# Kernel optimization log

Hardware: AMD Instinct MI355X
Metric: run time of the kernel (lower is better)

## Reference

```python
import jax, jax.numpy as jnp
import numpy as np

B, C, H, W = 16, 512, 64, 64
WS = 16            # window size -> N = 256 tokens per window
NH = 16            # num heads, head_dim = 32
HD = C // NH
HID = int((4 * C * 0.5) / 64) * 64   # SwiGLU hidden = 1024
CPB = 512
EPS = 1e-5


def _rel_tables(ws):
    r = np.arange(-(ws - 1), ws, dtype=np.float32)
    tab = np.stack(np.meshgrid(r, r, indexing='ij'), axis=-1)  # (2ws-1,2ws-1,2)
    tab = tab / (ws - 1)
    tab = tab * 8.0
    tab = np.sign(tab) * np.log2(np.abs(tab) + 1.0) / np.log2(8.0)
    # relative position index (N,N)
    coords = np.stack(np.meshgrid(np.arange(ws), np.arange(ws), indexing='ij'))
    cf = coords.reshape(2, -1)
    rel = (cf[:, :, None] - cf[:, None, :]).transpose(1, 2, 0).astype(np.int64)
    rel[:, :, 0] += ws - 1
    rel[:, :, 1] += ws - 1
    rel[:, :, 0] *= 2 * ws - 1
    idx = rel.sum(-1)
    return tab.reshape(-1, 2), idx


def setup_inputs() -> dict:
    key = jax.random.key(0)
    ks = jax.random.split(key, 12)
    s = 0.02
    tab, idx = _rel_tables(WS)
    return {
        'x': jax.random.normal(ks[0], (B, C, H, W), jnp.float32),
        'rel_table': jnp.asarray(tab),
        'norm1_w': jnp.ones((C,), jnp.float32),
        'norm1_b': jnp.zeros((C,), jnp.float32),
        'norm2_w': jnp.ones((C,), jnp.float32),
        'norm2_b': jnp.zeros((C,), jnp.float32),
        'qkv_w': jax.random.normal(ks[1], (C, 3 * C), jnp.float32) * s,
        'proj_w': jax.random.normal(ks[2], (C, C), jnp.float32) * s,
        'cpb_w1': jax.random.normal(ks[3], (2, CPB), jnp.float32) * s,
        'cpb_b1': jnp.zeros((CPB,), jnp.float32),
        'cpb_w2': jax.random.normal(ks[4], (CPB, NH), jnp.float32) * s,
        'fc1_w': jax.random.normal(ks[5], (C, 2 * HID), jnp.float32) * s,
        'fc2_w': jax.random.normal(ks[6], (HID, C), jnp.float32) * s,
        'rel_index': jnp.asarray(idx),
    }


def _ln(x, w, b):
    m = jnp.mean(x, axis=-1, keepdims=True)
    v = jnp.mean(jnp.square(x - m), axis=-1, keepdims=True)
    return (x - m) * jax.lax.rsqrt(v + EPS) * w + b


def reference(x, rel_table, norm1_w, norm1_b, norm2_w, norm2_b, qkv_w, proj_w,
              cpb_w1, cpb_b1, cpb_w2, fc1_w, fc2_w, rel_index):
    ws, nh, hd = WS, NH, HD
    N = ws * ws
    # window partition: (B,C,H,W) -> (B*nW, N, C)
    xw = x.reshape(B, C, H // ws, ws, W // ws, ws)
    xw = xw.transpose(0, 2, 4, 3, 5, 1).reshape(-1, N, C)
    Bw = xw.shape[0]

    # --- window attention ---
    h = _ln(xw, norm1_w, norm1_b)
    qkv = (h @ qkv_w).reshape(Bw, N, 3, nh, hd).transpose(2, 0, 3, 1, 4)
    q, k, v = qkv[0], qkv[1], qkv[2]          # (Bw, nh, N, hd)
    attn = jnp.einsum('bhnd,bhmd->bhnm', q, k) * (hd ** -0.5)
    # Swin-v2 continuous position bias MLP + gather
    bias_tab = jax.nn.relu(rel_table @ cpb_w1 + cpb_b1) @ cpb_w2   # ((2ws-1)^2, nh)
    bias = bias_tab[rel_index]                 # (N, N, nh)
    bias = 16.0 * jax.nn.sigmoid(bias.transpose(2, 0, 1))          # (nh, N, N)
    attn = jax.nn.softmax(attn + bias[None], axis=-1)
    o = jnp.einsum('bhnm,bhmd->bhnd', attn, v)
    o = o.transpose(0, 2, 1, 3).reshape(Bw, N, C) @ proj_w
    xw = xw + o

    # --- SwiGLU MLP ---
    h2 = _ln(xw, norm2_w, norm2_b)
    u = h2 @ fc1_w
    val, gate = jnp.split(u, 2, axis=-1)       # Mlp/SwiGLU: chunk -> silu(gate)*x
    xw = xw + (jax.nn.silu(gate) * val) @ fc2_w

    # window reverse + outer skip
    xr = xw.reshape(B, H // ws, W // ws, ws, ws, C)
    xr = xr.transpose(0, 5, 1, 3, 2, 4).reshape(B, C, H, W)
    return xr + x
```

## Files before the change

### kernel.cpp

```cpp
#include <hip/hip_runtime.h>
#include <hip/hip_bf16.h>

typedef unsigned short u16;
typedef unsigned int u32;
typedef __attribute__((ext_vector_type(8))) u16 u16x8;
typedef __attribute__((ext_vector_type(4))) u16 u16x4;
typedef __attribute__((ext_vector_type(8))) short bf16x8;
typedef __attribute__((ext_vector_type(4))) float f32x4;

__device__ __forceinline__ u16 f2bf(float f) {
  u32 u = __float_as_uint(f);
  u += 0x7fffu + ((u >> 16) & 1u);
  return (u16)(u >> 16);
}
__device__ __forceinline__ float bf2f(u16 h) {
  return __uint_as_float(((u32)h) << 16);
}
__device__ __forceinline__ u16 cvt_bf(float f) {
  __hip_bfloat16 h(f);
  return __builtin_bit_cast(u16, h);
}
__device__ __forceinline__ bf16x8 ld_bf8(const u16* p) {
  return __builtin_bit_cast(bf16x8, *(const u16x8*)p);
}

#if __has_builtin(__builtin_amdgcn_exp2f)
#define EXP2(x) __builtin_amdgcn_exp2f(x)
#else
#define EXP2(x) exp2f(x)
#endif

typedef const void __attribute__((address_space(1)))* gas_t;
typedef void __attribute__((address_space(3)))* las_t;
#define GLOAD_LDS16(gp, lp) __builtin_amdgcn_global_load_lds((gas_t)(gp), (las_t)(lp), 16, 0, 0)

#define QSCALE 0.25503486f
#define BIAS_MUL 23.08312065f

__global__ void wtrans_kernel(const float* __restrict__ in, u16* __restrict__ out, int K, int N) {
  int idx = blockIdx.x * 256 + threadIdx.x;
  if (idx >= K * N) return;
  int n = idx / K, k = idx - n * K;
  out[idx] = f2bf(in[(size_t)k * N + n]);
}

__global__ void wtrans_fc1_kernel(const float* __restrict__ in, u16* __restrict__ out) {
  int idx = blockIdx.x * 256 + threadIdx.x;
  int n = idx >> 9, k = idx & 511;
  int i = ((n >> 5) << 4) | (n & 15);
  int gsel = (n >> 4) & 1;
  out[idx] = f2bf(in[(size_t)k * 2048 + i + gsel * 1024]);
}

__global__ void cpb_kernel(const float* __restrict__ rt, const float* __restrict__ w1,
                           const float* __restrict__ b1, const float* __restrict__ w2,
                           float* __restrict__ tab2) {
  __shared__ float hid[512];
  __shared__ float part[16][17];
  int tix = blockIdx.x;
  int t = threadIdx.x;
  float r0 = rt[tix * 2], r1 = rt[tix * 2 + 1];
  for (int j = t; j < 512; j += 256) {
    float v = r0 * w1[j] + r1 * w1[512 + j] + b1[j];
    hid[j] = v > 0.f ? v : 0.f;
  }
  __syncthreads();
  int hh = t & 15, seg = t >> 4;
  float acc = 0.f;
  for (int j = seg * 32; j < seg * 32 + 32; ++j) acc += hid[j] * w2[j * 16 + hh];
  part[seg][hh] = acc;
  __syncthreads();
  if (t < 16) {
    float s = 0.f;
    for (int g = 0; g < 16; ++g) s += part[g][t];
    tab2[t * 961 + tix] = BIAS_MUL / (1.f + __expf(-s)) - 23.0f;
  }
}

__global__ __launch_bounds__(256, 2) void ln1_kernel(
    const float* __restrict__ x, const float* __restrict__ w, const float* __restrict__ b,
    u16* __restrict__ hbuf, u16* __restrict__ xwbuf) {
  __shared__ u16 tile[512 * 33];
  __shared__ float red[2][8][32];
  __shared__ float meanv[32], rstdv[32];
  int bi = blockIdx.x;
  int bimg = bi >> 7, rest = bi & 127, hrow = rest >> 1, half = rest & 1;
  int t = threadIdx.x, p = t & 31, g = t >> 5;
  const float* xr = x + (size_t)bimg * 512 * 4096 + (size_t)hrow * 64 + half * 32;
  float s = 0.f, s2 = 0.f;
  for (int i = 0; i < 64; ++i) {
    int c = g * 64 + i;
    float v = xr[(size_t)c * 4096 + p];
    tile[c * 33 + p] = f2bf(v);
    s += v; s2 += v * v;
  }
  red[0][g][p] = s; red[1][g][p] = s2;
  __syncthreads();
  if (t < 32) {
    float ss = 0.f, qq = 0.f;
    for (int gg = 0; gg < 8; ++gg) { ss += red[0][gg][t]; qq += red[1][gg][t]; }
    float mu = ss * (1.f / 512.f);
    float var = qq * (1.f / 512.f) - mu * mu;
    meanv[t] = mu;
    rstdv[t] = rsqrtf(var + 1e-5f);
  }
  __syncthreads();
  int c0 = t * 2;
  float w0 = w[c0], w1v = w[c0 + 1], b0 = b[c0], b1v = b[c0 + 1];
  int hy = hrow >> 4, iy = hrow & 15;
  for (int pp = 0; pp < 32; ++pp) {
    int pixel = half * 32 + pp;
    int wx = pixel >> 4, ix = pixel & 15;
    int widx = bimg * 16 + hy * 4 + wx;
    size_t basep = ((size_t)widx * 256 + iy * 16 + ix) * 512;
    u16 rb0 = tile[c0 * 33 + pp], rb1 = tile[(c0 + 1) * 33 + pp];
    float mu = meanv[pp], rs = rstdv[pp];
    float v0 = bf2f(rb0), v1 = bf2f(rb1);
    *(u32*)(xwbuf + basep + c0) = (u32)rb0 | ((u32)rb1 << 16);
    u16 h0 = f2bf((v0 - mu) * rs * w0 + b0);
    u16 h1 = f2bf((v1 - mu) * rs * w1v + b1v);
    *(u32*)(hbuf + basep + c0) = (u32)h0 | ((u32)h1 << 16);
  }
}

template <int EPI>
__global__ __launch_bounds__(256, 4) void gemm_bt(
    const u16* __restrict__ A, const u16* __restrict__ Bt,
    u16* __restrict__ out, const u16* __restrict__ res,
    u16* __restrict__ q_o, u16* __restrict__ k_o, u16* __restrict__ v_o,
    int M, int N, int K) {
  __shared__ u16 As[128 * 64];
  __shared__ u16 Bs[128 * 64];
  const int t = threadIdx.x, l = t & 63, wv = t >> 6;
  const int nbx = N >> 7;
  const int wg = (int)blockIdx.x;
  const int xcd = wg & 7, c = wg >> 3;
  const int cm = c / nbx;
  const int m0 = (xcd * 64 + cm) * 128, n0 = (c - cm * nbx) * 128;
  const int wr = wv >> 1, wc = wv & 1;
  const int lr = l & 15, lk = l >> 4;
  f32x4 acc[4][4] = {};
  for (int kt = 0; kt < K; kt += 64) {
#pragma unroll
    for (int j = 0; j < 4; ++j) {
      int qi = j * 256 + t;
      int r = qi >> 3, c8 = (qi & 7) * 8;
      GLOAD_LDS16(A + (size_t)(m0 + r) * K + kt + c8, As + (size_t)(j * 256 + wv * 64) * 8);
    }
#pragma unroll
    for (int j = 0; j < 4; ++j) {
      int qi = j * 256 + t;
      int r = qi >> 3, c8 = (qi & 7) * 8;
      GLOAD_LDS16(Bt + (size_t)(n0 + r) * K + kt + c8, Bs + (size_t)(j * 256 + wv * 64) * 8);
    }
    __syncthreads();
#pragma unroll
    for (int ks = 0; ks < 2; ++ks) {
      bf16x8 a[4], bb[4];
#pragma unroll
      for (int mf = 0; mf < 4; ++mf)
        a[mf] = ld_bf8(As + (wr * 64 + mf * 16 + lr) * 64 + ks * 32 + lk * 8);
#pragma unroll
      for (int nf = 0; nf < 4; ++nf)
        bb[nf] = ld_bf8(Bs + (wc * 64 + nf * 16 + lr) * 64 + ks * 32 + lk * 8);
#pragma unroll
      for (int mf = 0; mf < 4; ++mf)
#pragma unroll
        for (int nf = 0; nf < 4; ++nf)
          acc[mf][nf] = __builtin_amdgcn_mfma_f32_16x16x32_bf16(a[mf], bb[nf], acc[mf][nf], 0, 0, 0);
    }
    __syncthreads();
  }
#pragma unroll
  for (int mf = 0; mf < 4; ++mf) {
    int rbase = m0 + wr * 64 + mf * 16 + lk * 4;
    if constexpr (EPI == 3) {
#pragma unroll
      for (int nf = 0; nf < 4; nf += 2) {
        int colv = n0 + wc * 64 + nf * 16 + lr;
        int i = ((colv >> 5) << 4) | (colv & 15);
#pragma unroll
        for (int jj = 0; jj < 4; ++jj) {
          int row = rbase + jj;
          float val = acc[mf][nf][jj], gate = acc[mf][nf + 1][jj];
          float sil = gate / (1.f + __expf(-gate));
          out[(size_t)row * 1024 + i] = f2bf(sil * val);
        }
      }
    } else {
#pragma unroll
      for (int nf = 0; nf < 4; ++nf) {
        int col = n0 + wc * 64 + nf * 16 + lr;
#pragma unroll
        for (int jj = 0; jj < 4; ++jj) {
          int row = rbase + jj;
          float v = acc[mf][nf][jj];
          if constexpr (EPI == 0) {
            out[(size_t)row * N + col] = f2bf(v);
          } else if constexpr (EPI == 1) {
            out[(size_t)row * N + col] = f2bf(v + bf2f(res[(size_t)row * N + col]));
          } else if constexpr (EPI == 2) {
            int which = col >> 9, rem = col & 511;
            int hh = rem >> 5, dd = rem & 31;
            size_t dst = (((size_t)(row >> 8) * 16 + hh) * 256 + (size_t)(row & 255)) * 32 + dd;
            u16* po = which == 0 ? q_o : (which == 1 ? k_o : v_o);
            float sc = which == 0 ? QSCALE : 1.f;
            po[dst] = f2bf(v * sc);
          }
        }
      }
    }
  }
}

__global__ __launch_bounds__(256, 4) void attn_kernel(
    const u16* __restrict__ qb, const u16* __restrict__ kb, const u16* __restrict__ vb,
    const float* __restrict__ tab2, u16* __restrict__ ob) {
  __shared__ u16 vt[32 * 72];
  __shared__ float tabh4[31 * 32 * 4];
  __shared__ u16 pl[4][16 * 76];
  const int w = blockIdx.x, h = blockIdx.y;
  const int t = threadIdx.x, l = t & 63, wid = t >> 6;
  const size_t base = (size_t)(w * 16 + h) * 256 * 32;
  const u16* qg = qb + base;
  const u16* kg = kb + base;
  const u16* vg = vb + base;
  const float* th = tab2 + h * 961;
  for (int i = t; i < 992; i += 256) {
    int dy = i >> 5, dx = i & 31;
#pragma unroll
    for (int r = 0; r < 4; ++r) {
      int dxr = dx + r;
      tabh4[i * 4 + r] = (dxr <= 30) ? th[dy * 31 + dxr] : 0.f;
    }
  }
  const int q4 = l >> 4, c0 = l & 15;
  const int dx0 = q4 * 4 - c0 + 15;
  bf16x8 qa[4];
#pragma unroll
  for (int mf = 0; mf < 4; ++mf)
    qa[mf] = ld_bf8(qg + (wid * 64 + mf * 16 + c0) * 32 + q4 * 8);
  f32x4 oacc[4][2] = {};
  float psum[4][4] = {};
  for (int ct = 0; ct < 4; ++ct) {
    {
      int r = t & 63, j = t >> 6;
      u16x8 dv = *(const u16x8*)(vg + (ct * 64 + r) * 32 + j * 8);
#pragma unroll
      for (int e = 0; e < 8; ++e) vt[(j * 8 + e) * 72 + r] = dv[e];
    }
    __syncthreads();
    bf16x8 bfr[4];
#pragma unroll
    for (int nf = 0; nf < 4; ++nf)
      bfr[nf] = ld_bf8(kg + (ct * 64 + nf * 16 + c0) * 32 + q4 * 8);
    bf16x8 vfr[2][2];
#pragma unroll
    for (int df = 0; df < 2; ++df)
#pragma unroll
      for (int ks2 = 0; ks2 < 2; ++ks2)
        vfr[df][ks2] = ld_bf8(vt + (df * 16 + c0) * 72 + ks2 * 32 + q4 * 8);
#pragma unroll
    for (int mf = 0; mf < 4; ++mf) {
      f32x4 sacc[4] = {};
      __builtin_amdgcn_s_setprio(1);
#pragma unroll
      for (int nf = 0; nf < 4; ++nf)
        sacc[nf] = __builtin_amdgcn_mfma_f32_16x16x32_bf16(qa[mf], bfr[nf], sacc[nf], 0, 0, 0);
      __builtin_amdgcn_s_setprio(0);
      const int dyb = wid * 4 + mf - ct * 4 + 15;
#pragma unroll
      for (int nf = 0; nf < 4; ++nf) {
        f32x4 bv = *(const f32x4*)&tabh4[((dyb - nf) * 32 + dx0) * 4];
#pragma unroll
        for (int jj = 0; jj < 4; ++jj) {
          float p = EXP2(sacc[nf][jj] + bv[jj]);
          psum[mf][jj] += p;
          pl[wid][(q4 * 4 + jj) * 76 + nf * 16 + c0] = cvt_bf(p);
        }
      }
      __builtin_amdgcn_s_setprio(1);
#pragma unroll
      for (int ks2 = 0; ks2 < 2; ++ks2) {
        bf16x8 pa = ld_bf8(&pl[wid][c0 * 76 + ks2 * 32 + q4 * 8]);
        oacc[mf][0] = __builtin_amdgcn_mfma_f32_16x16x32_bf16(pa, vfr[0][ks2], oacc[mf][0], 0, 0, 0);
        oacc[mf][1] = __builtin_amdgcn_mfma_f32_16x16x32_bf16(pa, vfr[1][ks2], oacc[mf][1], 0, 0, 0);
      }
      __builtin_amdgcn_s_setprio(0);
    }
    __syncthreads();
  }
#pragma unroll
  for (int mf = 0; mf < 4; ++mf) {
#pragma unroll
    for (int jj = 0; jj < 4; ++jj) {
      float s = psum[mf][jj];
      s += __shfl_xor(s, 1);
      s += __shfl_xor(s, 2);
      s += __shfl_xor(s, 4);
      s += __shfl_xor(s, 8);
      float inv = 1.f / s;
      int row = wid * 64 + mf * 16 + q4 * 4 + jj;
      size_t obase = ((size_t)w * 256 + row) * 512 + h * 32;
      ob[obase + c0] = f2bf(oacc[mf][0][jj] * inv);
      ob[obase + 16 + c0] = f2bf(oacc[mf][1][jj] * inv);
    }
  }
}

__global__ __launch_bounds__(256, 4) void ln2_kernel(const u16* __restrict__ r1,
    const float* __restrict__ w, const float* __restrict__ b, u16* __restrict__ h2) {
  int t = threadIdx.x, l = t & 63, wid = t >> 6;
  size_t token = (size_t)blockIdx.x * 4 + wid;
  const u16* rp = r1 + token * 512 + l * 8;
  u16x8 raw = *(const u16x8*)rp;
  float v[8]; float s = 0.f, s2 = 0.f;
#pragma unroll
  for (int i = 0; i < 8; ++i) { v[i] = bf2f(raw[i]); s += v[i]; s2 += v[i] * v[i]; }
#pragma unroll
  for (int m = 1; m < 64; m <<= 1) { s += __shfl_xor(s, m); s2 += __shfl_xor(s2, m); }
  float mu = s * (1.f / 512.f);
  float var = s2 * (1.f / 512.f) - mu * mu;
  float rs = rsqrtf(var + 1e-5f);
  u16x8 o;
#pragma unroll
  for (int i = 0; i < 8; ++i) {
    int c = l * 8 + i;
    o[i] = f2bf((v[i] - mu) * rs * w[c] + b[c]);
  }
  *(u16x8*)(h2 + token * 512 + l * 8) = o;
}

__global__ __launch_bounds__(256, 2) void final_kernel(const u16* __restrict__ r2,
    const float* __restrict__ x, float* __restrict__ out) {
  __shared__ u16 tl[64 * 132];
  int cc = blockIdx.x;
  int hrow = blockIdx.y;
  int bimg = blockIdx.z;
  int t = threadIdx.x;
  int p = t >> 2, cp = t & 3;
  int hy = hrow >> 4, iy = hrow & 15;
  {
    int wx = p >> 4, ix = p & 15;
    size_t token = (size_t)(bimg * 16 + hy * 4 + wx) * 256 + iy * 16 + ix;
    const u16* rp = r2 + token * 512 + cc * 128 + cp * 32;
#pragma unroll
    for (int i = 0; i < 4; ++i) {
      u16x8 d = *(const u16x8*)(rp + i * 8);
      *(u16x4*)(tl + p * 132 + cp * 32 + i * 8) = *(u16x4*)&d;
      *(u16x4*)(tl + p * 132 + cp * 32 + i * 8 + 4) = *((u16x4*)&d + 1);
    }
  }
  __syncthreads();
  int p2 = t & 63, cg = t >> 6;
  size_t pbase = (size_t)bimg * 512 * 4096 + (size_t)(cc * 128) * 4096 + (size_t)hrow * 64 + p2;
  const float* xp = x + pbase;
  float* op = out + pbase;
#pragma unroll
  for (int i = 0; i < 32; ++i) {
    int cl = cg * 32 + i;
    op[(size_t)cl * 4096] = bf2f(tl[p2 * 132 + cl]) + xp[(size_t)cl * 4096];
  }
}

extern "C" void kernel_launch(void* const* d_in, const int* in_sizes, int n_in,
                              void* d_out, int out_size, void* d_ws, size_t ws_size,
                              hipStream_t stream) {
  (void)in_sizes; (void)n_in; (void)out_size; (void)ws_size;
  const float* x = (const float*)d_in[0];
  const float* rel_table = (const float*)d_in[1];
  const float* n1w = (const float*)d_in[2];
  const float* n1b = (const float*)d_in[3];
  const float* n2w = (const float*)d_in[4];
  const float* n2b = (const float*)d_in[5];
  const float* qkv_w = (const float*)d_in[6];
  const float* proj_w = (const float*)d_in[7];
  const float* cpb_w1 = (const float*)d_in[8];
  const float* cpb_b1 = (const float*)d_in[9];
  const float* cpb_w2 = (const float*)d_in[10];
  const float* fc1_w = (const float*)d_in[11];
  const float* fc2_w = (const float*)d_in[12];
  float* outp = (float*)d_out;
  char* ws = (char*)d_ws;

  u16* wq = (u16*)(ws + 0);
  u16* wp = (u16*)(ws + 1572864);
  u16* w1 = (u16*)(ws + 2097152);
  u16* w2 = (u16*)(ws + 4194304);
  float* tab2 = (float*)(ws + 5242880);
  const size_t RB = 67108864;
  u16* R0 = (u16*)(ws + 8388608);
  u16* R1 = (u16*)(ws + 8388608 + RB);
  u16* R2 = (u16*)(ws + 8388608 + 2 * RB);
  u16* R3 = (u16*)(ws + 8388608 + 3 * RB);
  u16* R4 = (u16*)(ws + 8388608 + 4 * RB);
  u16* R5 = (u16*)(ws + 8388608 + 5 * RB);

  wtrans_kernel<<<3072, 256, 0, stream>>>(qkv_w, wq, 512, 1536);
  wtrans_kernel<<<1024, 256, 0, stream>>>(proj_w, wp, 512, 512);
  wtrans_fc1_kernel<<<4096, 256, 0, stream>>>(fc1_w, w1);
  wtrans_kernel<<<2048, 256, 0, stream>>>(fc2_w, w2, 1024, 512);
  cpb_kernel<<<961, 256, 0, stream>>>(rel_table, cpb_w1, cpb_b1, cpb_w2, tab2);
  ln1_kernel<<<2048, 256, 0, stream>>>(x, n1w, n1b, R2, R0);
  gemm_bt<2><<<6144, 256, 0, stream>>>(R2, wq, nullptr, nullptr,
                                       R3, R4, R5, 65536, 1536, 512);
  attn_kernel<<<dim3(256, 16), 256, 0, stream>>>(R3, R4, R5, tab2, R2);
  gemm_bt<1><<<2048, 256, 0, stream>>>(R2, wp, R1, R0,
                                       nullptr, nullptr, nullptr, 65536, 512, 512);
  ln2_kernel<<<16384, 256, 0, stream>>>(R1, n2w, n2b, R3);
  gemm_bt<3><<<8192, 256, 0, stream>>>(R3, w1, R4, nullptr,
                                       nullptr, nullptr, nullptr, 65536, 2048, 512);
  gemm_bt<1><<<2048, 256, 0, stream>>>(R4, w2, R0, R1,
                                       nullptr, nullptr, nullptr, 65536, 512, 1024);
  final_kernel<<<dim3(4, 64, 16), 256, 0, stream>>>(R0, x, outp);
}
```

Before: 806.9 us.

## Add double-buffered LDS GEMM for fc1 SwiGLU and raise attention occupancy

Introduces a new gemm_db kernel that stages A and B tiles into two LDS buffers with direct global-to-LDS loads, prefetching the tile two steps ahead while computing on the current one. It uses partial vmcnt waits and raised MFMA priority, and is used only for the fc1 GEMM with the fused SwiGLU epilogue. The attention kernel's launch bounds also change from 4 to 5 waves per SIMD hint. The extra LDS (64KB per block) limits occupancy to about 2 blocks per CU, and the tighter register cap on attention could cause spills.

```diff
diff --git a/kernel.cpp b/kernel.cpp
--- a/kernel.cpp
+++ b/kernel.cpp
@@ -213,7 +213,106 @@
   }
 }
 
-__global__ __launch_bounds__(256, 4) void attn_kernel(
+template <int EPI>
+__global__ __launch_bounds__(256, 2) void gemm_db(
+    const u16* __restrict__ A, const u16* __restrict__ Bt,
+    u16* __restrict__ out, const u16* __restrict__ res,
+    int M, int N, int K) {
+  __shared__ u16 As[2][128 * 64];
+  __shared__ u16 Bs[2][128 * 64];
+  const int t = threadIdx.x, l = t & 63, wv = t >> 6;
+  const int nbx = N >> 7;
+  const int wg = (int)blockIdx.x;
+  const int xcd = wg & 7, c = wg >> 3;
+  const int cm = c / nbx;
+  const int m0 = (xcd * 64 + cm) * 128, n0 = (c - cm * nbx) * 128;
+  const int wr = wv >> 1, wc = wv & 1;
+  const int lr = l & 15, lk = l >> 4;
+  const int nt = K >> 6;
+
+  auto stage = [&](int b, int kt) {
+#pragma unroll
+    for (int j = 0; j < 4; ++j) {
+      int qi = j * 256 + t;
+      int r = qi >> 3, c8 = (qi & 7) * 8;
+      GLOAD_LDS16(A + (size_t)(m0 + r) * K + kt + c8, &As[b][(size_t)(j * 256 + wv * 64) * 8]);
+    }
+#pragma unroll
+    for (int j = 0; j < 4; ++j) {
+      int qi = j * 256 + t;
+      int r = qi >> 3, c8 = (qi & 7) * 8;
+      GLOAD_LDS16(Bt + (size_t)(n0 + r) * K + kt + c8, &Bs[b][(size_t)(j * 256 + wv * 64) * 8]);
+    }
+  };
+
+  f32x4 acc[4][4] = {};
+  stage(0, 0);
+  stage(1, 64);
+  for (int tt = 0; tt < nt; ++tt) {
+    if (tt + 1 < nt)
+      asm volatile("s_waitcnt vmcnt(8)" ::: "memory");
+    else
+      asm volatile("s_waitcnt vmcnt(0)" ::: "memory");
+    __builtin_amdgcn_s_barrier();
+    const u16* as = &As[tt & 1][0];
+    const u16* bs = &Bs[tt & 1][0];
+#pragma unroll
+    for (int ks = 0; ks < 2; ++ks) {
+      bf16x8 a[4], bb[4];
+#pragma unroll
+      for (int mf = 0; mf < 4; ++mf)
+        a[mf] = ld_bf8(as + (wr * 64 + mf * 16 + lr) * 64 + ks * 32 + lk * 8);
+#pragma unroll
+      for (int nf = 0; nf < 4; ++nf)
+        bb[nf] = ld_bf8(bs + (wc * 64 + nf * 16 + lr) * 64 + ks * 32 + lk * 8);
+      __builtin_amdgcn_s_setprio(1);
+#pragma unroll
+      for (int mf = 0; mf < 4; ++mf)
+#pragma unroll
+        for (int nf = 0; nf < 4; ++nf)
+          acc[mf][nf] = __builtin_amdgcn_mfma_f32_16x16x32_bf16(a[mf], bb[nf], acc[mf][nf], 0, 0, 0);
+      __builtin_amdgcn_s_setprio(0);
+    }
+    asm volatile("s_waitcnt lgkmcnt(0)" ::: "memory");
+    __builtin_amdgcn_s_barrier();
+    if (tt + 2 < nt) stage(tt & 1, (tt + 2) * 64);
+  }
+#pragma unroll
+  for (int mf = 0; mf < 4; ++mf) {
+    int rbase = m0 + wr * 64 + mf * 16 + lk * 4;
+    if constexpr (EPI == 3) {
+#pragma unroll
+      for (int nf = 0; nf < 4; nf += 2) {
+        int colv = n0 + wc * 64 + nf * 16 + lr;
+        int i = ((colv >> 5) << 4) | (colv & 15);
+#pragma unroll
+        for (int jj = 0; jj < 4; ++jj) {
+          int row = rbase + jj;
+          float val = acc[mf][nf][jj], gate = acc[mf][nf + 1][jj];
+          float sil = gate / (1.f + __expf(-gate));
+          out[(size_t)row * 1024 + i] = f2bf(sil * val);
+        }
+      }
+    } else {
+#pragma unroll
+      for (int nf = 0; nf < 4; ++nf) {
+        int col = n0 + wc * 64 + nf * 16 + lr;
+#pragma unroll
+        for (int jj = 0; jj < 4; ++jj) {
+          int row = rbase + jj;
+          float v = acc[mf][nf][jj];
+          if constexpr (EPI == 0) {
+            out[(size_t)row * N + col] = f2bf(v);
+          } else if constexpr (EPI == 1) {
+            out[(size_t)row * N + col] = f2bf(v + bf2f(res[(size_t)row * N + col]));
+          }
+        }
+      }
+    }
+  }
+}
+
+__global__ __launch_bounds__(256, 5) void attn_kernel(
     const u16* __restrict__ qb, const u16* __restrict__ kb, const u16* __restrict__ vb,
     const float* __restrict__ tab2, u16* __restrict__ ob) {
   __shared__ u16 vt[32 * 72];
@@ -408,8 +507,7 @@
   gemm_bt<1><<<2048, 256, 0, stream>>>(R2, wp, R1, R0,
                                        nullptr, nullptr, nullptr, 65536, 512, 512);
   ln2_kernel<<<16384, 256, 0, stream>>>(R1, n2w, n2b, R3);
-  gemm_bt<3><<<8192, 256, 0, stream>>>(R3, w1, R4, nullptr,
-                                       nullptr, nullptr, nullptr, 65536, 2048, 512);
+  gemm_db<3><<<8192, 256, 0, stream>>>(R3, w1, R4, nullptr, 65536, 2048, 512);
   gemm_bt<1><<<2048, 256, 0, stream>>>(R4, w2, R0, R1,
                                        nullptr, nullptr, nullptr, 65536, 512, 1024);
   final_kernel<<<dim3(4, 64, 16), 256, 0, stream>>>(R0, x, outp);
```

Result: slower. 1.015 ms (+25.8%).

## Fuse window-reverse and outer skip into fc2 GEMM epilogue; preload bias into MFMA accumulator

Applied to the files above, without the earlier changes.

The final fc2 GEMM now writes fp32 output directly in NCHW layout, adding both the MLP residual and the original input x. This removes the separate final_kernel and its bf16 round-trip through an intermediate buffer. The attention kernel now initialises the score accumulators with the position-bias values, so one add per element is dropped after the MFMA. The fused epilogue does strided per-column writes that may coalesce poorly, and ln1's launch bounds are raised to allow more waves per SIMD.

```diff
diff --git a/kernel.cpp b/kernel.cpp
--- a/kernel.cpp
+++ b/kernel.cpp
@@ -77,7 +77,7 @@
   }
 }
 
-__global__ __launch_bounds__(256, 2) void ln1_kernel(
+__global__ __launch_bounds__(256, 4) void ln1_kernel(
     const float* __restrict__ x, const float* __restrict__ w, const float* __restrict__ b,
     u16* __restrict__ hbuf, u16* __restrict__ xwbuf) {
   __shared__ u16 tile[512 * 33];
@@ -128,6 +128,7 @@
     const u16* __restrict__ A, const u16* __restrict__ Bt,
     u16* __restrict__ out, const u16* __restrict__ res,
     u16* __restrict__ q_o, u16* __restrict__ k_o, u16* __restrict__ v_o,
+    const float* __restrict__ xg, float* __restrict__ outf,
     int M, int N, int K) {
   __shared__ u16 As[128 * 64];
   __shared__ u16 Bs[128 * 64];
@@ -186,6 +187,19 @@
           float sil = gate / (1.f + __expf(-gate));
           out[(size_t)row * 1024 + i] = f2bf(sil * val);
         }
+      }
+    } else if constexpr (EPI == 4) {
+      int widx = rbase >> 8, iy = (rbase >> 4) & 15, ix0 = rbase & 15;
+      int bimg = widx >> 4, hy = (widx >> 2) & 3, wx = widx & 3;
+#pragma unroll
+      for (int nf = 0; nf < 4; ++nf) {
+        int col = n0 + wc * 64 + nf * 16 + lr;
+        size_t obase = (((size_t)(bimg * 512 + col) * 64) + hy * 16 + iy) * 64 + wx * 16 + ix0;
+        const float* xp = xg + obase;
+        float* op = outf + obase;
+#pragma unroll
+        for (int jj = 0; jj < 4; ++jj)
+          op[jj] = acc[mf][nf][jj] + bf2f(res[(size_t)(rbase + jj) * 512 + col]) + xp[jj];
       }
     } else {
 #pragma unroll
@@ -262,19 +276,21 @@
         vfr[df][ks2] = ld_bf8(vt + (df * 16 + c0) * 72 + ks2 * 32 + q4 * 8);
 #pragma unroll
     for (int mf = 0; mf < 4; ++mf) {
-      f32x4 sacc[4] = {};
+      const int dyb = wid * 4 + mf - ct * 4 + 15;
+      f32x4 sacc[4];
+#pragma unroll
+      for (int nf = 0; nf < 4; ++nf)
+        sacc[nf] = *(const f32x4*)&tabh4[((dyb - nf) * 32 + dx0) * 4];
       __builtin_amdgcn_s_setprio(1);
 #pragma unroll
       for (int nf = 0; nf < 4; ++nf)
         sacc[nf] = __builtin_amdgcn_mfma_f32_16x16x32_bf16(qa[mf], bfr[nf], sacc[nf], 0, 0, 0);
       __builtin_amdgcn_s_setprio(0);
-      const int dyb = wid * 4 + mf - ct * 4 + 15;
 #pragma unroll
       for (int nf = 0; nf < 4; ++nf) {
-        f32x4 bv = *(const f32x4*)&tabh4[((dyb - nf) * 32 + dx0) * 4];
 #pragma unroll
         for (int jj = 0; jj < 4; ++jj) {
-          float p = EXP2(sacc[nf][jj] + bv[jj]);
+          float p = EXP2(sacc[nf][jj]);
           psum[mf][jj] += p;
           pl[wid][(q4 * 4 + jj) * 76 + nf * 16 + c0] = cvt_bf(p);
         }
@@ -329,38 +345,6 @@
     o[i] = f2bf((v[i] - mu) * rs * w[c] + b[c]);
   }
   *(u16x8*)(h2 + token * 512 + l * 8) = o;
-}
-
-__global__ __launch_bounds__(256, 2) void final_kernel(const u16* __restrict__ r2,
-    const float* __restrict__ x, float* __restrict__ out) {
-  __shared__ u16 tl[64 * 132];
-  int cc = blockIdx.x;
-  int hrow = blockIdx.y;
-  int bimg = blockIdx.z;
-  int t = threadIdx.x;
-  int p = t >> 2, cp = t & 3;
-  int hy = hrow >> 4, iy = hrow & 15;
-  {
-    int wx = p >> 4, ix = p & 15;
-    size_t token = (size_t)(bimg * 16 + hy * 4 + wx) * 256 + iy * 16 + ix;
-    const u16* rp = r2 + token * 512 + cc * 128 + cp * 32;
-#pragma unroll
-    for (int i = 0; i < 4; ++i) {
-      u16x8 d = *(const u16x8*)(rp + i * 8);
-      *(u16x4*)(tl + p * 132 + cp * 32 + i * 8) = *(u16x4*)&d;
-      *(u16x4*)(tl + p * 132 + cp * 32 + i * 8 + 4) = *((u16x4*)&d + 1);
-    }
-  }
-  __syncthreads();
-  int p2 = t & 63, cg = t >> 6;
-  size_t pbase = (size_t)bimg * 512 * 4096 + (size_t)(cc * 128) * 4096 + (size_t)hrow * 64 + p2;
-  const float* xp = x + pbase;
-  float* op = out + pbase;
-#pragma unroll
-  for (int i = 0; i < 32; ++i) {
-    int cl = cg * 32 + i;
-    op[(size_t)cl * 4096] = bf2f(tl[p2 * 132 + cl]) + xp[(size_t)cl * 4096];
-  }
 }
 
 extern "C" void kernel_launch(void* const* d_in, const int* in_sizes, int n_in,
@@ -403,14 +387,13 @@
   cpb_kernel<<<961, 256, 0, stream>>>(rel_table, cpb_w1, cpb_b1, cpb_w2, tab2);
   ln1_kernel<<<2048, 256, 0, stream>>>(x, n1w, n1b, R2, R0);
   gemm_bt<2><<<6144, 256, 0, stream>>>(R2, wq, nullptr, nullptr,
-                                       R3, R4, R5, 65536, 1536, 512);
+                                       R3, R4, R5, nullptr, nullptr, 65536, 1536, 512);
   attn_kernel<<<dim3(256, 16), 256, 0, stream>>>(R3, R4, R5, tab2, R2);
   gemm_bt<1><<<2048, 256, 0, stream>>>(R2, wp, R1, R0,
-                                       nullptr, nullptr, nullptr, 65536, 512, 512);
+                                       nullptr, nullptr, nullptr, nullptr, nullptr, 65536, 512, 512);
   ln2_kernel<<<16384, 256, 0, stream>>>(R1, n2w, n2b, R3);
   gemm_bt<3><<<8192, 256, 0, stream>>>(R3, w1, R4, nullptr,
-                                       nullptr, nullptr, nullptr, 65536, 2048, 512);
-  gemm_bt<1><<<2048, 256, 0, stream>>>(R4, w2, R0, R1,
-                                       nullptr, nullptr, nullptr, 65536, 512, 1024);
-  final_kernel<<<dim3(4, 64, 16), 256, 0, stream>>>(R0, x, outp);
-}
+                                       nullptr, nullptr, nullptr, nullptr, nullptr, 65536, 2048, 512);
+  gemm_bt<4><<<2048, 256, 0, stream>>>(R4, w2, nullptr, R1,
+                                       nullptr, nullptr, nullptr, x, outp, 65536, 512, 1024);
+}
```

After: 759.3 us. 1.06x faster.
